# Optimization experiments

Hardware: AMD Instinct MI355X
Metric: run time of the kernel (lower is better)

## Reference

```python
import jax, jax.numpy as jnp
import numpy as np

N_NODES = 100000
N_EDGES = 800000
NODE_IN = 32
EDGE_DIM = 84
HIDDEN = 24
HEAD_HIDDEN = 20
DEPTH = 2
CAT = 2 * HIDDEN + EDGE_DIM  # 132
LN_EPS = 1e-5


def _gelu(x):
    # torch nn.GELU default = exact erf form
    return jax.nn.gelu(x, approximate=False)


def _ln(x, g, b):
    m = jnp.mean(x, axis=-1, keepdims=True)
    v = jnp.var(x, axis=-1, keepdims=True)
    return (x - m) * jax.lax.rsqrt(v + LN_EPS) * g + b


def setup_inputs() -> dict:
    key = jax.random.key(0)
    ks = jax.random.split(key, 32)
    f = jnp.float32

    def nrm(k, shape, scale=0.05):
        return jax.random.normal(k, shape, dtype=f) * scale

    inp = {
        "x": jax.random.normal(ks[0], (N_NODES, NODE_IN), dtype=f),
        "edge_attr": jax.random.normal(ks[1], (N_EDGES, EDGE_DIM), dtype=f),
        # input projection
        "node_w": nrm(ks[2], (NODE_IN, HIDDEN)),
        "node_b": jnp.zeros((HIDDEN,), f),
        # intrinsic head
        "ih_w1": nrm(ks[3], (HIDDEN, HEAD_HIDDEN)),
        "ih_b1": jnp.zeros((HEAD_HIDDEN,), f),
        "ih_w2": nrm(ks[4], (HEAD_HIDDEN, 1)),
        "ih_b2": jnp.zeros((1,), f),
        # per-layer phi_e (stacked over depth)
        "pe_w1": nrm(ks[5], (DEPTH, CAT, EDGE_DIM)),
        "pe_b1": jnp.zeros((DEPTH, EDGE_DIM), f),
        "pe_w2": nrm(ks[6], (DEPTH, EDGE_DIM, EDGE_DIM)),
        "pe_b2": jnp.zeros((DEPTH, EDGE_DIM), f),
        # per-layer phi_v
        "pv_w1": nrm(ks[7], (DEPTH, CAT, HIDDEN)),
        "pv_b1": jnp.zeros((DEPTH, HIDDEN), f),
        "pv_w2": nrm(ks[8], (DEPTH, HIDDEN, HIDDEN)),
        "pv_b2": jnp.zeros((DEPTH, HIDDEN), f),
        # layer norms
        "ne_g": jnp.ones((DEPTH, EDGE_DIM), f),
        "ne_b": jnp.zeros((DEPTH, EDGE_DIM), f),
        "nv_g": jnp.ones((DEPTH, HIDDEN), f),
        "nv_b": jnp.zeros((DEPTH, HIDDEN), f),
        # context head
        "ch_w1": nrm(ks[9], (HIDDEN, HEAD_HIDDEN)),
        "ch_b1": jnp.zeros((HEAD_HIDDEN,), f),
        "ch_w2": nrm(ks[10], (HEAD_HIDDEN, 1)),
        "ch_b2": jnp.zeros((1,), f),
        "mu": jnp.zeros((), f),
        "edge_index": jax.random.randint(ks[11], (2, N_EDGES), 0, N_NODES),
    }
    return inp


def reference(x, edge_attr, node_w, node_b, ih_w1, ih_b1, ih_w2, ih_b2,
              pe_w1, pe_b1, pe_w2, pe_b2, pv_w1, pv_b1, pv_w2, pv_b2,
              ne_g, ne_b, nv_g, nv_b, ch_w1, ch_b1, ch_w2, ch_b2, mu,
              edge_index):
    src, dst = edge_index[0], edge_index[1]
    n = x.shape[0]
    # eval mode: dropout and edge_drop are inactive
    h = x @ node_w + node_b                                   # [N, H]
    intrinsic = (_gelu(h @ ih_w1 + ih_b1) @ ih_w2 + ih_b2)[:, 0]
    e = edge_attr                                             # [E, De]
    ones = jnp.ones((src.shape[0], 1), dtype=x.dtype)
    counts = jnp.maximum(jax.ops.segment_sum(ones, dst, num_segments=n), 1.0)
    for i in range(DEPTH):
        hs, hd = h[src], h[dst]                               # gathers [E, H]
        cat = jnp.concatenate([hs, hd, e], axis=-1)           # [E, 132]
        e_msg = _gelu(cat @ pe_w1[i] + pe_b1[i]) @ pe_w2[i] + pe_b2[i]
        e = _ln(e + e_msg, ne_g[i], ne_b[i])
        cat = jnp.concatenate([hs, hd, e], axis=-1)
        m = _gelu(cat @ pv_w1[i] + pv_b1[i]) @ pv_w2[i] + pv_b2[i]
        agg = jax.ops.segment_sum(m, dst, num_segments=n) / counts  # scatter-mean
        h = _ln(h + agg, nv_g[i], nv_b[i])
    context = (_gelu(h @ ch_w1 + ch_b1) @ ch_w2 + ch_b2)[:, 0]
    return mu + intrinsic + context
```

## Files before the change

kernel.cpp:

```cpp
#include <hip/hip_runtime.h>
#include <math.h>

#define N_NODES 100000
#define N_EDGES 800000
#define NODE_IN 32
#define EDGE_DIM 84
#define HIDDEN 24
#define HEAD_HIDDEN 20
#define CAT_DIM 132
#define LN_EPS 1e-5f

typedef __attribute__((ext_vector_type(8))) short short8;
typedef __attribute__((ext_vector_type(4))) float f32x4;
typedef unsigned int uint;
typedef unsigned short ushort;

__device__ __forceinline__ float gelu_exact(float x) {
    return 0.5f * x * (1.0f + erff(x * 0.70710678118654752f));
}
__device__ __forceinline__ ushort f2bf(float f) {
    union { float f; uint u; } c; c.f = f;
    uint u = c.u;
    return (ushort)((u + 0x7fffu + ((u >> 16) & 1u)) >> 16);
}
__device__ __forceinline__ float bf2f(ushort s) {
    union { uint u; float f; } c; c.u = ((uint)s) << 16; return c.f;
}

__global__ void k_prep_w(const float* __restrict__ pe_w1, const float* __restrict__ pe_w2,
                         const float* __restrict__ pv_w1, const float* __restrict__ pv_w2,
                         ushort* __restrict__ wp) {
    int idx = blockIdx.x * 256 + threadIdx.x;
    int j = idx & 7;
    int lane = (idx >> 3) & 63;
    int frag = idx >> 9;
    int kq = (lane >> 4) * 8 + j;
    int n15 = lane & 15;
    float v = 0.f;
    if (frag < 60) {
        int l = frag / 30, f = frag % 30;
        int kt = f / 6, nt = f % 6;
        int k = kt * 32 + kq, n = nt * 16 + n15;
        if (k < CAT_DIM && n < EDGE_DIM) v = pe_w1[(l * CAT_DIM + k) * EDGE_DIM + n];
    } else if (frag < 96) {
        int f2 = frag - 60; int l = f2 / 18, f = f2 % 18;
        int kt = f / 6, nt = f % 6;
        int k = kt * 32 + kq, n = nt * 16 + n15;
        if (k < EDGE_DIM && n < EDGE_DIM) v = pe_w2[(l * EDGE_DIM + k) * EDGE_DIM + n];
    } else if (frag < 116) {
        int f2 = frag - 96; int l = f2 / 10, f = f2 % 10;
        int kt = f / 2, nt = f % 2;
        int k = kt * 32 + kq, n = nt * 16 + n15;
        if (k < CAT_DIM && n < HIDDEN) v = pv_w1[(l * CAT_DIM + k) * HIDDEN + n];
    } else {
        int f2 = frag - 116; int l = f2 / 2, nt = f2 % 2;
        int k = kq, n = nt * 16 + n15;
        if (k < HIDDEN && n < HIDDEN) v = pv_w2[(l * HIDDEN + k) * HIDDEN + n];
    }
    wp[idx] = f2bf(v);
}

__global__ void k_node_in(const float* __restrict__ x,
                          const float* __restrict__ node_w, const float* __restrict__ node_b,
                          const float* __restrict__ ih_w1, const float* __restrict__ ih_b1,
                          const float* __restrict__ ih_w2, const float* __restrict__ ih_b2,
                          float* __restrict__ h, ushort* __restrict__ h_bf,
                          float* __restrict__ intr) {
    int n = blockIdx.x * blockDim.x + threadIdx.x;
    if (n >= N_NODES) return;
    float xv[NODE_IN];
    const float4* xp = (const float4*)(x + (size_t)n * NODE_IN);
#pragma unroll
    for (int i = 0; i < NODE_IN / 4; i++) {
        float4 v = xp[i];
        xv[4*i+0] = v.x; xv[4*i+1] = v.y; xv[4*i+2] = v.z; xv[4*i+3] = v.w;
    }
    float hv[HIDDEN];
#pragma unroll
    for (int j = 0; j < HIDDEN; j++) hv[j] = node_b[j];
    for (int k = 0; k < NODE_IN; k++) {
        float xk = xv[k];
#pragma unroll
        for (int j = 0; j < HIDDEN; j++) hv[j] = fmaf(xk, node_w[k * HIDDEN + j], hv[j]);
    }
#pragma unroll
    for (int j = 0; j < HIDDEN; j++) {
        h[(size_t)n * HIDDEN + j] = hv[j];
        h_bf[(size_t)n * HIDDEN + j] = f2bf(hv[j]);
    }
    float acc = ih_b2[0];
    for (int j = 0; j < HEAD_HIDDEN; j++) {
        float t = ih_b1[j];
#pragma unroll
        for (int k = 0; k < HIDDEN; k++) t = fmaf(hv[k], ih_w1[k * HEAD_HIDDEN + j], t);
        acc = fmaf(gelu_exact(t), ih_w2[j], acc);
    }
    intr[n] = acc;
}

__global__ void k_counts(const int* __restrict__ ei, int* __restrict__ cnt) {
    int e = blockIdx.x * blockDim.x + threadIdx.x;
    if (e >= N_EDGES) return;
    atomicAdd(&cnt[ei[N_EDGES + e]], 1);
}

__device__ __forceinline__ short8 ld_catA(const ushort* __restrict__ h_bf,
                                          const float* __restrict__ eattr,
                                          const ushort* __restrict__ e_bf,
                                          int src, int dst, long rowg, int c) {
    if (c < 48) {
        const ushort* p = (c < 24) ? h_bf + (size_t)src * 24 + c
                                   : h_bf + (size_t)dst * 24 + (c - 24);
        return *(const short8*)p;
    }
    int ec = c - 48;
    if (eattr) {
        const float* q = eattr + rowg * 84;
        f32x4 lo = *(const f32x4*)(q + ((ec <= 80) ? ec : 0));
        f32x4 hi = *(const f32x4*)(q + ((ec <= 76) ? (ec + 4) : 0));
        short8 r;
        r[0] = (short)f2bf(lo[0]); r[1] = (short)f2bf(lo[1]);
        r[2] = (short)f2bf(lo[2]); r[3] = (short)f2bf(lo[3]);
        r[4] = (short)f2bf(hi[0]); r[5] = (short)f2bf(hi[1]);
        r[6] = (short)f2bf(hi[2]); r[7] = (short)f2bf(hi[3]);
        return r;
    }
    return *(const short8*)(e_bf + rowg * 96 + ((ec < 96) ? ec : 0));
}

__device__ __forceinline__ short8 ld_catV(const ushort* __restrict__ h_bf,
                                          const ushort* __restrict__ sT,
                                          int src, int dst, int rowL, int c) {
    if (c < 48) {
        const ushort* p = (c < 24) ? h_bf + (size_t)src * 24 + c
                                   : h_bf + (size_t)dst * 24 + (c - 24);
        return *(const short8*)p;
    }
    int ec = c - 48;
    return *(const short8*)(sT + rowL * 104 + ((ec < 96) ? ec : 0));
}

__global__ __launch_bounds__(256, 8)
void k_edge_fused(const ushort* __restrict__ h_bf,
                  const float* __restrict__ eattr,
                  ushort* __restrict__ e_bf,
                  const int* __restrict__ ei,
                  const ushort* __restrict__ w1f, const ushort* __restrict__ w2f,
                  const ushort* __restrict__ v1f, const ushort* __restrict__ v2f,
                  const float* __restrict__ b1, const float* __restrict__ b2,
                  const float* __restrict__ g, const float* __restrict__ bb,
                  const float* __restrict__ vb1, const float* __restrict__ vb2,
                  float* __restrict__ agg, int store_e) {
    __shared__ __align__(16) ushort sT[64 * 104];
    __shared__ __align__(16) ushort sTV[64 * 40];
    __shared__ int s_idx[128];

    const int tid = threadIdx.x;
    const int e0 = blockIdx.x * 64;
    if (tid < 128) s_idx[tid] = ei[(size_t)(tid >> 6) * N_EDGES + e0 + (tid & 63)];
    __syncthreads();

    const int lane = tid & 63, wave = tid >> 6;
    const int quad = lane >> 4, l15 = lane & 15;
    const int cbase = quad * 8;
    const int rA = wave * 16 + l15;
    const int srcA = s_idx[rA], dstA = s_idx[64 + rA];

    f32x4 acc[6];
#pragma unroll
    for (int nt = 0; nt < 6; nt++) acc[nt] = (f32x4)0.f;
#pragma unroll
    for (int kt = 0; kt < 5; kt++) {
        int c = kt * 32 + cbase;
        short8 a = ld_catA(h_bf, eattr, e_bf, srcA, dstA, (long)(e0 + rA), c);
        const short8* bp = (const short8*)w1f + kt * 6 * 64 + lane;
#pragma unroll
        for (int nt = 0; nt < 6; nt++) {
            short8 b = bp[nt * 64];
            acc[nt] = __builtin_amdgcn_mfma_f32_16x16x32_bf16(a, b, acc[nt], 0, 0, 0);
        }
    }
#pragma unroll
    for (int nt = 0; nt < 6; nt++) {
        int col = nt * 16 + l15;
        float bv = (col < EDGE_DIM) ? b1[col] : 0.f;
#pragma unroll
        for (int r = 0; r < 4; r++) {
            int row = wave * 16 + quad * 4 + r;
            sT[row * 104 + col] = f2bf(gelu_exact(acc[nt][r] + bv));
        }
    }

    f32x4 acc2[6];
#pragma unroll
    for (int nt = 0; nt < 6; nt++) acc2[nt] = (f32x4)0.f;
#pragma unroll
    for (int kt = 0; kt < 3; kt++) {
        short8 a = *(const short8*)(sT + (size_t)rA * 104 + kt * 32 + cbase);
        const short8* bp = (const short8*)w2f + kt * 6 * 64 + lane;
#pragma unroll
        for (int nt = 0; nt < 6; nt++) {
            short8 b = bp[nt * 64];
            acc2[nt] = __builtin_amdgcn_mfma_f32_16x16x32_bf16(a, b, acc2[nt], 0, 0, 0);
        }
    }

#pragma unroll
    for (int r = 0; r < 4; r++) {
        int row = wave * 16 + quad * 4 + r;
        long rg = e0 + row;
        float vv[6];
        float ss = 0.f, qq = 0.f;
#pragma unroll
        for (int nt = 0; nt < 6; nt++) {
            int col = nt * 16 + l15;
            float v = 0.f;
            if (col < EDGE_DIM) {
                v = acc2[nt][r] + b2[col];
                v += eattr ? eattr[rg * 84 + col] : bf2f(e_bf[rg * 96 + col]);
            }
            vv[nt] = v; ss += v; qq = fmaf(v, v, qq);
        }
        ss += __shfl_xor(ss, 1); ss += __shfl_xor(ss, 2);
        ss += __shfl_xor(ss, 4); ss += __shfl_xor(ss, 8);
        qq += __shfl_xor(qq, 1); qq += __shfl_xor(qq, 2);
        qq += __shfl_xor(qq, 4); qq += __shfl_xor(qq, 8);
        float mean = ss * (1.f / EDGE_DIM);
        float var  = qq * (1.f / EDGE_DIM) - mean * mean;
        float rstd = rsqrtf(var + LN_EPS);
#pragma unroll
        for (int nt = 0; nt < 6; nt++) {
            int col = nt * 16 + l15;
            if (col < EDGE_DIM)
                sT[row * 104 + col] = f2bf((vv[nt] - mean) * rstd * g[col] + bb[col]);
        }
    }

    f32x4 av[2];
#pragma unroll
    for (int nt = 0; nt < 2; nt++) av[nt] = (f32x4)0.f;
#pragma unroll
    for (int kt = 0; kt < 5; kt++) {
        int c = kt * 32 + cbase;
        short8 a = ld_catV(h_bf, sT, srcA, dstA, rA, c);
        const short8* bp = (const short8*)v1f + kt * 2 * 64 + lane;
#pragma unroll
        for (int nt = 0; nt < 2; nt++) {
            short8 b = bp[nt * 64];
            av[nt] = __builtin_amdgcn_mfma_f32_16x16x32_bf16(a, b, av[nt], 0, 0, 0);
        }
    }
#pragma unroll
    for (int nt = 0; nt < 2; nt++) {
        int col = nt * 16 + l15;
        float bv = (col < HIDDEN) ? vb1[col] : 0.f;
#pragma unroll
        for (int r = 0; r < 4; r++) {
            int row = wave * 16 + quad * 4 + r;
            sTV[row * 40 + col] = f2bf(gelu_exact(av[nt][r] + bv));
        }
    }

    f32x4 av2[2];
#pragma unroll
    for (int nt = 0; nt < 2; nt++) av2[nt] = (f32x4)0.f;
    {
        short8 a = *(const short8*)(sTV + (size_t)rA * 40 + cbase);
        const short8* bp = (const short8*)v2f + lane;
#pragma unroll
        for (int nt = 0; nt < 2; nt++) {
            short8 b = bp[nt * 64];
            av2[nt] = __builtin_amdgcn_mfma_f32_16x16x32_bf16(a, b, av2[nt], 0, 0, 0);
        }
    }
#pragma unroll
    for (int nt = 0; nt < 2; nt++) {
        int col = nt * 16 + l15;
        if (col < HIDDEN) {
            float bv = vb2[col];
#pragma unroll
            for (int r = 0; r < 4; r++) {
                int row = wave * 16 + quad * 4 + r;
                int d = s_idx[64 + row];
                atomicAdd(&agg[(size_t)d * HIDDEN + col], av2[nt][r] + bv);
            }
        }
    }

    if (store_e) {
        __syncthreads();
        const uint* sTu = (const uint*)sT;
        uint* dst32 = (uint*)e_bf + (size_t)e0 * 48;
#pragma unroll
        for (int i = 0; i < 12; i++) {
            int idx = tid + 256 * i;
            int row = idx / 48, d = idx - row * 48;
            dst32[idx] = sTu[row * 52 + d];
        }
    }
}

__global__ void k_node_up(float* __restrict__ h, ushort* __restrict__ h_bf,
                          const float* __restrict__ agg,
                          const int* __restrict__ cnt,
                          const float* __restrict__ g, const float* __restrict__ b) {
    int n = blockIdx.x * blockDim.x + threadIdx.x;
    if (n >= N_NODES) return;
    int c = cnt[n]; if (c < 1) c = 1;
    float inv = 1.0f / (float)c;
    float v[HIDDEN];
    float s = 0.f;
#pragma unroll
    for (int j = 0; j < HIDDEN; j++) {
        v[j] = h[(size_t)n * HIDDEN + j] + agg[(size_t)n * HIDDEN + j] * inv;
        s += v[j];
    }
    float mean = s * (1.f / HIDDEN);
    float sq = 0.f;
#pragma unroll
    for (int j = 0; j < HIDDEN; j++) { float d = v[j] - mean; sq = fmaf(d, d, sq); }
    float rstd = rsqrtf(sq * (1.f / HIDDEN) + LN_EPS);
#pragma unroll
    for (int j = 0; j < HIDDEN; j++) {
        float o = (v[j] - mean) * rstd * g[j] + b[j];
        h[(size_t)n * HIDDEN + j] = o;
        h_bf[(size_t)n * HIDDEN + j] = f2bf(o);
    }
}

__global__ void k_final(const float* __restrict__ h, const float* __restrict__ intr,
                        const float* __restrict__ ch_w1, const float* __restrict__ ch_b1,
                        const float* __restrict__ ch_w2, const float* __restrict__ ch_b2,
                        const float* __restrict__ mu, float* __restrict__ out) {
    int n = blockIdx.x * blockDim.x + threadIdx.x;
    if (n >= N_NODES) return;
    float hv[HIDDEN];
#pragma unroll
    for (int j = 0; j < HIDDEN; j++) hv[j] = h[(size_t)n * HIDDEN + j];
    float acc = ch_b2[0];
    for (int j = 0; j < HEAD_HIDDEN; j++) {
        float t = ch_b1[j];
#pragma unroll
        for (int k = 0; k < HIDDEN; k++) t = fmaf(hv[k], ch_w1[k * HEAD_HIDDEN + j], t);
        acc = fmaf(gelu_exact(t), ch_w2[j], acc);
    }
    out[n] = mu[0] + intr[n] + acc;
}

extern "C" void kernel_launch(void* const* d_in, const int* in_sizes, int n_in,
                              void* d_out, int out_size, void* d_ws, size_t ws_size,
                              hipStream_t stream) {
    const float* x        = (const float*)d_in[0];
    const float* edge_attr= (const float*)d_in[1];
    const float* node_w   = (const float*)d_in[2];
    const float* node_b   = (const float*)d_in[3];
    const float* ih_w1    = (const float*)d_in[4];
    const float* ih_b1    = (const float*)d_in[5];
    const float* ih_w2    = (const float*)d_in[6];
    const float* ih_b2    = (const float*)d_in[7];
    const float* pe_w1    = (const float*)d_in[8];
    const float* pe_b1    = (const float*)d_in[9];
    const float* pe_w2    = (const float*)d_in[10];
    const float* pe_b2    = (const float*)d_in[11];
    const float* pv_w1    = (const float*)d_in[12];
    const float* pv_b1    = (const float*)d_in[13];
    const float* pv_w2    = (const float*)d_in[14];
    const float* pv_b2    = (const float*)d_in[15];
    const float* ne_g     = (const float*)d_in[16];
    const float* ne_b     = (const float*)d_in[17];
    const float* nv_g     = (const float*)d_in[18];
    const float* nv_b     = (const float*)d_in[19];
    const float* ch_w1    = (const float*)d_in[20];
    const float* ch_b1    = (const float*)d_in[21];
    const float* ch_w2    = (const float*)d_in[22];
    const float* ch_b2    = (const float*)d_in[23];
    const float* mu       = (const float*)d_in[24];
    const int*   ei       = (const int*)d_in[25];

    char* ws = (char*)d_ws;
    float*  h    = (float*)ws;  ws += (size_t)N_NODES * HIDDEN * 4;
    float*  agg  = (float*)ws;  ws += (size_t)N_NODES * HIDDEN * 4;
    float*  intr = (float*)ws;  ws += (size_t)N_NODES * 4;
    int*    cnt  = (int*)ws;    ws += (size_t)N_NODES * 4;
    ushort* h_bf = (ushort*)ws; ws += (size_t)N_NODES * HIDDEN * 2;
    ushort* wp   = (ushort*)ws; ws += (size_t)61440 * 2;
    ws = (char*)(((size_t)ws + 255) & ~(size_t)255);
    ushort* e_bf = (ushort*)ws; ws += (size_t)N_EDGES * 96 * 2;

    const ushort* we1[2] = { wp + 0 * 15360, wp + 1 * 15360 };
    const ushort* we2[2] = { wp + 30720 + 0 * 9216, wp + 30720 + 1 * 9216 };
    const ushort* wv1[2] = { wp + 49152 + 0 * 5120, wp + 49152 + 1 * 5120 };
    const ushort* wv2[2] = { wp + 59392 + 0 * 1024, wp + 59392 + 1 * 1024 };

    hipMemsetAsync(cnt, 0, (size_t)N_NODES * 4, stream);
    k_prep_w<<<240, 256, 0, stream>>>(pe_w1, pe_w2, pv_w1, pv_w2, wp);
    k_counts<<<(N_EDGES + 255) / 256, 256, 0, stream>>>(ei, cnt);
    k_node_in<<<(N_NODES + 255) / 256, 256, 0, stream>>>(
        x, node_w, node_b, ih_w1, ih_b1, ih_w2, ih_b2, h, h_bf, intr);

    const int eb = N_EDGES / 64;
    for (int L = 0; L < 2; L++) {
        hipMemsetAsync(agg, 0, (size_t)N_NODES * HIDDEN * 4, stream);
        k_edge_fused<<<eb, 256, 0, stream>>>(
            h_bf, (L == 0) ? edge_attr : (const float*)nullptr, e_bf, ei,
            we1[L], we2[L], wv1[L], wv2[L],
            pe_b1 + (size_t)L * EDGE_DIM, pe_b2 + (size_t)L * EDGE_DIM,
            ne_g + (size_t)L * EDGE_DIM, ne_b + (size_t)L * EDGE_DIM,
            pv_b1 + (size_t)L * HIDDEN, pv_b2 + (size_t)L * HIDDEN,
            agg, (L == 0) ? 1 : 0);
        k_node_up<<<(N_NODES + 255) / 256, 256, 0, stream>>>(
            h, h_bf, agg, cnt, nv_g + (size_t)L * HIDDEN, nv_b + (size_t)L * HIDDEN);
    }
    k_final<<<(N_NODES + 255) / 256, 256, 0, stream>>>(
        h, intr, ch_w1, ch_b1, ch_w2, ch_b2, mu, (float*)d_out);
}
```

Baseline: 1.137 ms.

## Stage concatenated edge inputs in shared memory and shrink stored edge row stride

Result: faster. 1.052 ms (-7.5%).

```diff
diff --git a/kernel.cpp b/kernel.cpp
--- a/kernel.cpp
+++ b/kernel.cpp
@@ -11,6 +11,7 @@
 #define LN_EPS 1e-5f
 
 typedef __attribute__((ext_vector_type(8))) short short8;
+typedef __attribute__((ext_vector_type(4))) short bfx4;
 typedef __attribute__((ext_vector_type(4))) float f32x4;
 typedef unsigned int uint;
 typedef unsigned short ushort;
@@ -104,42 +105,6 @@
     atomicAdd(&cnt[ei[N_EDGES + e]], 1);
 }
 
-__device__ __forceinline__ short8 ld_catA(const ushort* __restrict__ h_bf,
-                                          const float* __restrict__ eattr,
-                                          const ushort* __restrict__ e_bf,
-                                          int src, int dst, long rowg, int c) {
-    if (c < 48) {
-        const ushort* p = (c < 24) ? h_bf + (size_t)src * 24 + c
-                                   : h_bf + (size_t)dst * 24 + (c - 24);
-        return *(const short8*)p;
-    }
-    int ec = c - 48;
-    if (eattr) {
-        const float* q = eattr + rowg * 84;
-        f32x4 lo = *(const f32x4*)(q + ((ec <= 80) ? ec : 0));
-        f32x4 hi = *(const f32x4*)(q + ((ec <= 76) ? (ec + 4) : 0));
-        short8 r;
-        r[0] = (short)f2bf(lo[0]); r[1] = (short)f2bf(lo[1]);
-        r[2] = (short)f2bf(lo[2]); r[3] = (short)f2bf(lo[3]);
-        r[4] = (short)f2bf(hi[0]); r[5] = (short)f2bf(hi[1]);
-        r[6] = (short)f2bf(hi[2]); r[7] = (short)f2bf(hi[3]);
-        return r;
-    }
-    return *(const short8*)(e_bf + rowg * 96 + ((ec < 96) ? ec : 0));
-}
-
-__device__ __forceinline__ short8 ld_catV(const ushort* __restrict__ h_bf,
-                                          const ushort* __restrict__ sT,
-                                          int src, int dst, int rowL, int c) {
-    if (c < 48) {
-        const ushort* p = (c < 24) ? h_bf + (size_t)src * 24 + c
-                                   : h_bf + (size_t)dst * 24 + (c - 24);
-        return *(const short8*)p;
-    }
-    int ec = c - 48;
-    return *(const short8*)(sT + rowL * 104 + ((ec < 96) ? ec : 0));
-}
-
 __global__ __launch_bounds__(256, 8)
 void k_edge_fused(const ushort* __restrict__ h_bf,
                   const float* __restrict__ eattr,
@@ -151,28 +116,63 @@
                   const float* __restrict__ g, const float* __restrict__ bb,
                   const float* __restrict__ vb1, const float* __restrict__ vb2,
                   float* __restrict__ agg, int store_e) {
-    __shared__ __align__(16) ushort sT[64 * 104];
+    __shared__ __align__(16) ushort sCat[64 * 136];
     __shared__ __align__(16) ushort sTV[64 * 40];
     __shared__ int s_idx[128];
 
     const int tid = threadIdx.x;
     const int e0 = blockIdx.x * 64;
+
     if (tid < 128) s_idx[tid] = ei[(size_t)(tid >> 6) * N_EDGES + e0 + (tid & 63)];
+#pragma unroll
+    for (int i = 0; i < 2; i++) {
+        int idx = tid + 256 * i;
+        if (idx < 384) {
+            int row = idx / 6, part = idx - row * 6;
+            int node = ei[(size_t)(part >= 3) * N_EDGES + e0 + row];
+            short8 v = *(const short8*)(h_bf + (size_t)node * 24 + (part % 3) * 8);
+            *(short8*)(sCat + row * 136 + part * 8) = v;
+        }
+    }
+    if (eattr) {
+#pragma unroll
+        for (int i = 0; i < 6; i++) {
+            int u = tid + 256 * i;
+            if (u < 1344) {
+                int row = u / 21, c4 = u - row * 21;
+                f32x4 v = *(const f32x4*)(eattr + (size_t)(e0 + row) * 84 + c4 * 4);
+                bfx4 w;
+                w[0] = (short)f2bf(v[0]); w[1] = (short)f2bf(v[1]);
+                w[2] = (short)f2bf(v[2]); w[3] = (short)f2bf(v[3]);
+                *(bfx4*)(sCat + row * 136 + 48 + c4 * 4) = w;
+            }
+        }
+        sCat[(tid >> 2) * 136 + 132 + (tid & 3)] = 0;
+    } else {
+#pragma unroll
+        for (int i = 0; i < 3; i++) {
+            int u = tid + 256 * i;
+            if (u < 704) {
+                int row = u / 11, c8 = u - row * 11;
+                *(short8*)(sCat + row * 136 + 48 + c8 * 8) =
+                    *(const short8*)(e_bf + (size_t)(e0 + row) * 88 + c8 * 8);
+            }
+        }
+    }
     __syncthreads();
 
     const int lane = tid & 63, wave = tid >> 6;
     const int quad = lane >> 4, l15 = lane & 15;
     const int cbase = quad * 8;
     const int rA = wave * 16 + l15;
-    const int srcA = s_idx[rA], dstA = s_idx[64 + rA];
 
     f32x4 acc[6];
 #pragma unroll
     for (int nt = 0; nt < 6; nt++) acc[nt] = (f32x4)0.f;
 #pragma unroll
     for (int kt = 0; kt < 5; kt++) {
-        int c = kt * 32 + cbase;
-        short8 a = ld_catA(h_bf, eattr, e_bf, srcA, dstA, (long)(e0 + rA), c);
+        int c = kt * 32 + cbase; if (c > 128) c = 128;
+        short8 a = *(const short8*)(sCat + rA * 136 + c);
         const short8* bp = (const short8*)w1f + kt * 6 * 64 + lane;
 #pragma unroll
         for (int nt = 0; nt < 6; nt++) {
@@ -187,7 +187,7 @@
 #pragma unroll
         for (int r = 0; r < 4; r++) {
             int row = wave * 16 + quad * 4 + r;
-            sT[row * 104 + col] = f2bf(gelu_exact(acc[nt][r] + bv));
+            if (col < 88) sCat[row * 136 + 48 + col] = f2bf(gelu_exact(acc[nt][r] + bv));
         }
     }
 
@@ -196,7 +196,8 @@
     for (int nt = 0; nt < 6; nt++) acc2[nt] = (f32x4)0.f;
 #pragma unroll
     for (int kt = 0; kt < 3; kt++) {
-        short8 a = *(const short8*)(sT + (size_t)rA * 104 + kt * 32 + cbase);
+        int c = kt * 32 + cbase; if (c > 80) c = 80;
+        short8 a = *(const short8*)(sCat + rA * 136 + 48 + c);
         const short8* bp = (const short8*)w2f + kt * 6 * 64 + lane;
 #pragma unroll
         for (int nt = 0; nt < 6; nt++) {
@@ -217,7 +218,7 @@
             float v = 0.f;
             if (col < EDGE_DIM) {
                 v = acc2[nt][r] + b2[col];
-                v += eattr ? eattr[rg * 84 + col] : bf2f(e_bf[rg * 96 + col]);
+                v += eattr ? eattr[rg * 84 + col] : bf2f(e_bf[rg * 88 + col]);
             }
             vv[nt] = v; ss += v; qq = fmaf(v, v, qq);
         }
@@ -232,7 +233,7 @@
         for (int nt = 0; nt < 6; nt++) {
             int col = nt * 16 + l15;
             if (col < EDGE_DIM)
-                sT[row * 104 + col] = f2bf((vv[nt] - mean) * rstd * g[col] + bb[col]);
+                sCat[row * 136 + 48 + col] = f2bf((vv[nt] - mean) * rstd * g[col] + bb[col]);
         }
     }
 
@@ -241,8 +242,8 @@
     for (int nt = 0; nt < 2; nt++) av[nt] = (f32x4)0.f;
 #pragma unroll
     for (int kt = 0; kt < 5; kt++) {
-        int c = kt * 32 + cbase;
-        short8 a = ld_catV(h_bf, sT, srcA, dstA, rA, c);
+        int c = kt * 32 + cbase; if (c > 128) c = 128;
+        short8 a = *(const short8*)(sCat + rA * 136 + c);
         const short8* bp = (const short8*)v1f + kt * 2 * 64 + lane;
 #pragma unroll
         for (int nt = 0; nt < 2; nt++) {
@@ -288,14 +289,14 @@
     }
 
     if (store_e) {
-        __syncthreads();
-        const uint* sTu = (const uint*)sT;
-        uint* dst32 = (uint*)e_bf + (size_t)e0 * 48;
-#pragma unroll
-        for (int i = 0; i < 12; i++) {
-            int idx = tid + 256 * i;
-            int row = idx / 48, d = idx - row * 48;
-            dst32[idx] = sTu[row * 52 + d];
+        const uint* sU = (const uint*)sCat;
+        uint* dst32 = (uint*)e_bf;
+#pragma unroll
+        for (int i = 0; i < 11; i++) {
+            int idx = lane + 64 * i;
+            int rl = idx / 44, d = idx - rl * 44;
+            int row = wave * 16 + rl;
+            dst32[(size_t)(e0 + row) * 44 + d] = sU[row * 68 + 24 + d];
         }
     }
 }
@@ -385,7 +386,7 @@
     ushort* h_bf = (ushort*)ws; ws += (size_t)N_NODES * HIDDEN * 2;
     ushort* wp   = (ushort*)ws; ws += (size_t)61440 * 2;
     ws = (char*)(((size_t)ws + 255) & ~(size_t)255);
-    ushort* e_bf = (ushort*)ws; ws += (size_t)N_EDGES * 96 * 2;
+    ushort* e_bf = (ushort*)ws; ws += (size_t)N_EDGES * 88 * 2;
 
     const ushort* we1[2] = { wp + 0 * 15360, wp + 1 * 15360 };
     const ushort* we2[2] = { wp + 30720 + 0 * 9216, wp + 30720 + 1 * 9216 };
```
